# Performance work log

Hardware: AMD Instinct MI355X
Metric: run time of the kernel (lower is better)

The kernel has to match this reference:

```python
import jax, jax.numpy as jnp
import numpy as np

VS = 0.4
SENT = np.int32(2_000_000_000)  # > max lin code (1000^3)
EPS = 1e-5


def setup_inputs() -> dict:
    key = jax.random.key(0)
    ks = jax.random.split(key, 16)
    B, N, Cin, Cout = 8, 65536, 16, 128
    xyz = jax.random.uniform(ks[0], (B, N, 3), jnp.float32) * 51.2  # 128^3 voxel grid @ 0.4m
    feat = jax.random.normal(ks[1], (B, N, Cin), jnp.float32)
    mask = (jax.random.uniform(ks[2], (B, N)) < 0.9).astype(jnp.float32)
    def conv_w(k, ci, co):
        return jax.random.normal(k, (27, ci, co), jnp.float32) * (1.0 / np.sqrt(27.0 * ci))
    return {
        'xyz': xyz, 'feat': feat, 'mask': mask,
        'W1': conv_w(ks[3], Cin, 32), 'b1': jnp.zeros((32,), jnp.float32),
        'g1': jnp.ones((32,), jnp.float32), 'be1': jnp.zeros((32,), jnp.float32),
        'W2': conv_w(ks[4], 32, 64), 'b2': jnp.zeros((64,), jnp.float32),
        'g2': jnp.ones((64,), jnp.float32), 'be2': jnp.zeros((64,), jnp.float32),
        'W3': conv_w(ks[5], 64, Cout), 'b3': jnp.zeros((Cout,), jnp.float32),
        'g3': jnp.ones((Cout,), jnp.float32), 'be3': jnp.zeros((Cout,), jnp.float32),
    }


def _voxelize(lin_b, f_b, m_b):
    # sort-based unique with inverse; fixed capacity N slots (sentinel-padded)
    N = lin_b.shape[0]
    order = jnp.argsort(lin_b)
    s = lin_b[order]
    isnew = jnp.concatenate([jnp.ones((1,), bool), s[1:] != s[:-1]])
    rank = (jnp.cumsum(isnew) - 1).astype(jnp.int32)
    inv = jnp.zeros_like(lin_b).at[order].set(rank)          # point -> voxel slot
    unq = jnp.full_like(lin_b, SENT).at[rank].set(s)         # sorted unique codes, sentinel fill
    fsum = jax.ops.segment_sum(f_b * m_b[:, None], inv, num_segments=N)
    cnt = jnp.clip(jax.ops.segment_sum(m_b, inv, num_segments=N), 1.0)
    return unq, inv, fsum / cnt[:, None]


def _subm_conv(vfeat, unq, valid, W, b):
    # submanifold 3x3x3 conv on active voxels; neighbor lookup via binary search in sorted codes
    B, N, _ = vfeat.shape
    x = unq % 1000
    y = (unq // 1000) % 1000
    z = unq // 1000000
    brow = jnp.arange(B)[:, None]
    out = jnp.zeros((B, N, W.shape[-1]), vfeat.dtype)
    for ko in range(27):
        dz, dy, dx = ko // 9 - 1, (ko // 3) % 3 - 1, ko % 3 - 1
        ncode = unq + dx + 1000 * dy + 1000000 * dz
        inb = ((x + dx >= 0) & (x + dx < 1000) & (y + dy >= 0) & (y + dy < 1000)
               & (z + dz >= 0) & (z + dz < 1000))
        idx = jnp.clip(jax.vmap(jnp.searchsorted)(unq, ncode), 0, N - 1)
        found = (jnp.take_along_axis(unq, idx, 1) == ncode) & inb & valid
        nf = vfeat[brow, idx] * found[..., None].astype(vfeat.dtype)
        out = out + nf @ W[ko]
    return (out + b) * valid[..., None].astype(vfeat.dtype)


def _bn_relu(xv, g, be, valid):
    # BatchNorm1d (training stats) over valid voxel rows only, then ReLU
    w = valid[..., None].astype(xv.dtype)
    n = jnp.maximum(w.sum(), 1.0)
    mean = (xv * w).sum((0, 1)) / n
    var = (((xv - mean) ** 2) * w).sum((0, 1)) / n
    yv = (xv - mean) * jax.lax.rsqrt(var + EPS) * g + be
    return jax.nn.relu(yv) * w


def reference(xyz, feat, mask, W1, b1, g1, be1, W2, b2, g2, be2, W3, b3, g3, be3):
    B, N, _ = feat.shape
    origin = xyz.reshape(-1, 3).min(0)
    v = jnp.clip(((xyz - origin) / VS).astype(jnp.int32), 0, None)   # [B,N,3]
    lin = v[..., 0] + 1000 * (v[..., 1] + 1000 * v[..., 2])          # [B,N]
    unq, inv, vfeat = jax.vmap(_voxelize)(lin, feat, mask)
    valid = unq < SENT
    h = _bn_relu(_subm_conv(vfeat, unq, valid, W1, b1), g1, be1, valid)
    h = _bn_relu(_subm_conv(h, unq, valid, W2, b2), g2, be2, valid)
    h = _bn_relu(_subm_conv(h, unq, valid, W3, b3), g3, be3, valid)
    # scatter voxel features back to points (exact match: inv maps point -> its voxel slot)
    out_f = h[jnp.arange(B)[:, None], inv]                           # [B,N,Cout]
    return out_f * mask[..., None]
```

## Files before the change

kernel.cpp:

```cpp
#include <hip/hip_runtime.h>

#define NPTS   65536
#define NBATCH 8
#define TSIZE  131072
#define TM1    (TSIZE - 1)
#define CAP    8192
#define PPB    64
#define BMW    65536
#define STG    64
#define PCS    16

__device__ __forceinline__ unsigned hashf(int code) {
    unsigned u = (unsigned)code * 2654435761u;
    return (u >> 13) & TM1;
}

__global__ void init_origin(int* ob) {
    if (threadIdx.x < 3) ob[threadIdx.x] = 0x7F800000;
}

__global__ void minred(const float* __restrict__ xyz, int* __restrict__ ob) {
    int tid = threadIdx.x;
    float mx = INFINITY, my = INFINITY, mz = INFINITY;
    size_t total = (size_t)NBATCH * NPTS;
    for (size_t i = (size_t)blockIdx.x * blockDim.x + tid; i < total;
         i += (size_t)gridDim.x * blockDim.x) {
        mx = fminf(mx, xyz[i * 3 + 0]);
        my = fminf(my, xyz[i * 3 + 1]);
        mz = fminf(mz, xyz[i * 3 + 2]);
    }
    __shared__ float sx[256], sy[256], sz[256];
    sx[tid] = mx; sy[tid] = my; sz[tid] = mz;
    __syncthreads();
    for (int s = 128; s > 0; s >>= 1) {
        if (tid < s) {
            sx[tid] = fminf(sx[tid], sx[tid + s]);
            sy[tid] = fminf(sy[tid], sy[tid + s]);
            sz[tid] = fminf(sz[tid], sz[tid + s]);
        }
        __syncthreads();
    }
    if (tid == 0) {
        atomicMin(&ob[0], __float_as_int(sx[0]));
        atomicMin(&ob[1], __float_as_int(sy[0]));
        atomicMin(&ob[2], __float_as_int(sz[0]));
    }
}

__global__ void build_codes(const float* __restrict__ xyz, const int* __restrict__ ob,
                            int* __restrict__ pslot, int* __restrict__ hashk,
                            int* __restrict__ scnt) {
    int b = blockIdx.y;
    int p = blockIdx.x * blockDim.x + threadIdx.x;
    size_t gi = (size_t)b * NPTS + p;
    float ox = __int_as_float(ob[0]);
    float oy = __int_as_float(ob[1]);
    float oz = __int_as_float(ob[2]);
    float x = xyz[gi * 3 + 0], y = xyz[gi * 3 + 1], z = xyz[gi * 3 + 2];
    int vx = (int)((x - ox) / 0.4f); if (vx < 0) vx = 0;
    int vy = (int)((y - oy) / 0.4f); if (vy < 0) vy = 0;
    int vz = (int)((z - oz) / 0.4f); if (vz < 0) vz = 0;
    int code = vx | (vy << 7) | (vz << 14);
    int* hk = hashk + (size_t)b * TSIZE;
    unsigned s = hashf(code);
    while (true) {
        int prev = atomicCAS(&hk[s], -1, code);
        if (prev == -1 || prev == code) break;
        s = (s + 1) & TM1;
    }
    pslot[gi] = (int)s;
    atomicAdd(&scnt[(size_t)b * TSIZE + s], 1);
}

__global__ void assign_ids(const int* __restrict__ hashk, int* __restrict__ hashv,
                           int* __restrict__ nvox, int* __restrict__ voxcode,
                           unsigned* __restrict__ bitmap, const int* __restrict__ scnt,
                           int* __restrict__ vnpts) {
    int b = blockIdx.y;
    int s = blockIdx.x * blockDim.x + threadIdx.x;
    int k = hashk[(size_t)b * TSIZE + s];
    if (k != -1) {
        int id = atomicAdd(&nvox[b], 1);
        hashv[(size_t)b * TSIZE + s] = id;
        voxcode[(size_t)b * NPTS + id] = k;
        vnpts[(size_t)b * NPTS + id] = scnt[(size_t)b * TSIZE + s];
        atomicOr(&bitmap[(size_t)b * BMW + (k >> 5)], 1u << (k & 31));
    }
}

__global__ void point_pass(const int* __restrict__ pslot, const int* __restrict__ scnt,
                           const int* __restrict__ hashv, const float* __restrict__ feat,
                           const float* __restrict__ mask, int* __restrict__ inv,
                           float* __restrict__ cntf, float* __restrict__ fsum) {
    int b = blockIdx.y;
    int p = blockIdx.x * blockDim.x + threadIdx.x;
    size_t gi = (size_t)b * NPTS + p;
    int s = pslot[gi];
    int v = hashv[(size_t)b * TSIZE + s];
    inv[gi] = v;
    int n = scnt[(size_t)b * TSIZE + s];
    float m = mask[gi];
    const float4* f4 = (const float4*)(feat + gi * 16);
    float4 f0 = f4[0], f1 = f4[1], f2 = f4[2], f3 = f4[3];
    float* fs = fsum + ((size_t)b * NPTS + v) * 16;
    if (n == 1) {
        float4 o0 = {f0.x * m, f0.y * m, f0.z * m, f0.w * m};
        float4 o1 = {f1.x * m, f1.y * m, f1.z * m, f1.w * m};
        float4 o2 = {f2.x * m, f2.y * m, f2.z * m, f2.w * m};
        float4 o3 = {f3.x * m, f3.y * m, f3.z * m, f3.w * m};
        float4* fs4 = (float4*)fs;
        fs4[0] = o0; fs4[1] = o1; fs4[2] = o2; fs4[3] = o3;
    } else {
        atomicAdd(&cntf[(size_t)b * NPTS + v], m);
        atomicAdd(&fs[0],  f0.x * m); atomicAdd(&fs[1],  f0.y * m);
        atomicAdd(&fs[2],  f0.z * m); atomicAdd(&fs[3],  f0.w * m);
        atomicAdd(&fs[4],  f1.x * m); atomicAdd(&fs[5],  f1.y * m);
        atomicAdd(&fs[6],  f1.z * m); atomicAdd(&fs[7],  f1.w * m);
        atomicAdd(&fs[8],  f2.x * m); atomicAdd(&fs[9],  f2.y * m);
        atomicAdd(&fs[10], f2.z * m); atomicAdd(&fs[11], f2.w * m);
        atomicAdd(&fs[12], f3.x * m); atomicAdd(&fs[13], f3.y * m);
        atomicAdd(&fs[14], f3.z * m); atomicAdd(&fs[15], f3.w * m);
    }
}

__global__ void vfeat_div(float* __restrict__ fsum, const float* __restrict__ cntf,
                          const int* __restrict__ vnpts, const int* __restrict__ nvox) {
    int b = blockIdx.y;
    int v = blockIdx.x * blockDim.x + threadIdx.x;
    if (v >= nvox[b]) return;
    if (vnpts[(size_t)b * NPTS + v] <= 1) return;
    float cn = fmaxf(cntf[(size_t)b * NPTS + v], 1.0f);
    float* fs = fsum + ((size_t)b * NPTS + v) * 16;
    #pragma unroll
    for (int c = 0; c < 16; c++) fs[c] /= cn;
}

__global__ __launch_bounds__(256) void build_pairs(
    const int* __restrict__ hashk, const int* __restrict__ hashv,
    const int* __restrict__ voxcode, const int* __restrict__ nvox,
    const unsigned* __restrict__ bitmap,
    unsigned* __restrict__ pairs, int* __restrict__ paircnt) {
    int b = blockIdx.y;
    int t = threadIdx.x;
    int v = blockIdx.x * 256 + t;
    __shared__ int lcnt[32];
    __shared__ int lbase[32];
    __shared__ unsigned s_pay[27 * STG];
    if (t < 32) lcnt[t] = 0;
    __syncthreads();

    bool active = (v < nvox[b]);
    int code = 0;
    if (active) code = voxcode[(size_t)b * NPTS + v];
    int x = code & 127, y = (code >> 7) & 127, z = code >> 14;
    const unsigned* bm = bitmap + (size_t)b * BMW;
    const int* hk = hashk + (size_t)b * TSIZE;
    const int* hv = hashv + (size_t)b * TSIZE;

    int ncode[13];
    unsigned hitmask = 0;
    #pragma unroll
    for (int d = 0; d < 13; d++) {
        int dz = d / 9 - 1, r9 = d % 9;
        int dy = r9 / 3 - 1, dx = r9 % 3 - 1;
        int nx = x + dx, ny = y + dy, nz = z + dz;
        bool inb = active && ((unsigned)nx <= 127u) && ((unsigned)ny <= 127u) &&
                   ((unsigned)nz <= 127u);
        int nc = nx | (ny << 7) | (nz << 14);
        ncode[d] = nc;
        unsigned w = 0;
        if (inb) w = bm[nc >> 5];
        if (inb && ((w >> (nc & 31)) & 1u)) hitmask |= 1u << d;
    }

    #pragma unroll
    for (int d = 0; d < 13; d++) {
        if (hitmask & (1u << d)) {
            int nc = ncode[d];
            unsigned s = hashf(nc);
            int nb = -1;
            while (true) {
                int k = hk[s];
                if (k == nc) { nb = hv[s]; break; }
                if (k == -1) break;
                s = (s + 1) & TM1;
            }
            if (nb >= 0) {
                unsigned p1 = ((unsigned)v << 16) | (unsigned)nb;
                unsigned p2 = ((unsigned)nb << 16) | (unsigned)v;
                int l1 = atomicAdd(&lcnt[d], 1);
                if (l1 < STG) {
                    s_pay[d * STG + l1] = p1;
                } else {
                    int gs = atomicAdd(&paircnt[(b * 27 + d) * PCS], 1);
                    if (gs < CAP) pairs[(size_t)(b * 27 + d) * CAP + gs] = p1;
                }
                int k2 = 26 - d;
                int l2 = atomicAdd(&lcnt[k2], 1);
                if (l2 < STG) {
                    s_pay[k2 * STG + l2] = p2;
                } else {
                    int gs = atomicAdd(&paircnt[(b * 27 + k2) * PCS], 1);
                    if (gs < CAP) pairs[(size_t)(b * 27 + k2) * CAP + gs] = p2;
                }
            }
        }
    }
    __syncthreads();

    if (t < 27) {
        int n = lcnt[t]; if (n > STG) n = STG;
        lbase[t] = (n > 0) ? atomicAdd(&paircnt[(b * 27 + t) * PCS], n) : 0;
    }
    __syncthreads();

    for (int k = t; k < 27 * STG; k += 256) {
        int bkt = k / STG, i = k % STG;
        int n = lcnt[bkt]; if (n > STG) n = STG;
        if (i < n) {
            int gs = lbase[bkt] + i;
            if (gs < CAP) pairs[(size_t)(b * 27 + bkt) * CAP + gs] = s_pay[k];
        }
    }
}

template <int Cin, int Cout, bool XFORM>
__global__ __launch_bounds__(256) void conv_center(
    const float* __restrict__ in, float* __restrict__ outp,
    const float* __restrict__ W13, const float* __restrict__ bias,
    const float* __restrict__ sc, const float* __restrict__ sh,
    const int* __restrict__ nvox) {
    constexpr int BR  = 64;
    constexpr int CT  = (Cout < 64) ? Cout : 64;
    constexpr int RG  = 256 / CT;
    constexpr int RPT = BR / RG;
    constexpr int J   = Cout / CT;
    int b = blockIdx.y;
    int nv = nvox[b];
    int v0 = blockIdx.x * BR;
    if (v0 >= nv) return;
    __shared__ __align__(16) float A_s[Cin][BR + 4];
    __shared__ __align__(16) float W_s[Cin * Cout];
    int t = threadIdx.x;
    for (int i4 = t; i4 < Cin * Cout / 4; i4 += 256)
        ((float4*)W_s)[i4] = ((const float4*)W13)[i4];
    const float* inb = in + (size_t)b * NPTS * Cin;
    for (int i4 = t; i4 < BR * Cin / 4; i4 += 256) {
        int lin = i4 * 4;
        int r = lin / Cin, ci = lin % Cin;
        float4 val = *(const float4*)&inb[(size_t)(v0 + r) * Cin + ci];
        if (XFORM) {
            val.x = fmaxf(val.x * sc[ci + 0] + sh[ci + 0], 0.0f);
            val.y = fmaxf(val.y * sc[ci + 1] + sh[ci + 1], 0.0f);
            val.z = fmaxf(val.z * sc[ci + 2] + sh[ci + 2], 0.0f);
            val.w = fmaxf(val.w * sc[ci + 3] + sh[ci + 3], 0.0f);
        }
        A_s[ci + 0][r] = val.x;
        A_s[ci + 1][r] = val.y;
        A_s[ci + 2][r] = val.z;
        A_s[ci + 3][r] = val.w;
    }
    __syncthreads();
    int c = t % CT;
    int r0 = (t / CT) * RPT;
    float acc[RPT][J];
    #pragma unroll
    for (int r = 0; r < RPT; r++)
        #pragma unroll
        for (int j = 0; j < J; j++) acc[r][j] = 0.0f;
    #pragma unroll 4
    for (int ci = 0; ci < Cin; ci++) {
        float4 a4[RPT / 4];
        #pragma unroll
        for (int k = 0; k < RPT / 4; k++)
            a4[k] = *(const float4*)&A_s[ci][r0 + 4 * k];
        float w[J];
        #pragma unroll
        for (int j = 0; j < J; j++) w[j] = W_s[ci * Cout + c + CT * j];
        #pragma unroll
        for (int k = 0; k < RPT / 4; k++) {
            #pragma unroll
            for (int j = 0; j < J; j++) {
                acc[4 * k + 0][j] += a4[k].x * w[j];
                acc[4 * k + 1][j] += a4[k].y * w[j];
                acc[4 * k + 2][j] += a4[k].z * w[j];
                acc[4 * k + 3][j] += a4[k].w * w[j];
            }
        }
    }
    float* ob = outp + (size_t)b * NPTS * Cout;
    #pragma unroll
    for (int r = 0; r < RPT; r++) {
        int row = v0 + r0 + r;
        if (row < nv) {
            #pragma unroll
            for (int j = 0; j < J; j++)
                ob[(size_t)row * Cout + c + CT * j] = acc[r][j] + bias[c + CT * j];
        }
    }
}

template <int Cin, int Cout, bool XFORM>
__global__ __launch_bounds__(256) void conv_off(
    const float* __restrict__ in, float* __restrict__ outp,
    const float* __restrict__ W, const float* __restrict__ sc,
    const float* __restrict__ sh, const unsigned* __restrict__ pairs,
    const int* __restrict__ paircnt) {
    constexpr int BR  = PPB;
    constexpr int CT  = (Cout < 64) ? Cout : 64;
    constexpr int RG  = 256 / CT;
    constexpr int RPT = BR / RG;
    constexpr int J   = Cout / CT;
    int bk = blockIdx.y;
    int ko = bk % 27;
    int b  = bk / 27;
    int cnt = paircnt[bk * PCS];
    if (cnt > CAP) cnt = CAP;
    int start = blockIdx.x * BR;
    if (start >= cnt) return;
    int nActive = cnt - start; if (nActive > BR) nActive = BR;
    __shared__ __align__(16) float A_s[Cin][BR + 4];
    __shared__ __align__(16) float W_s[Cin * Cout];
    __shared__ unsigned pr_s[BR];
    int t = threadIdx.x;
    const float* Wk = W + (size_t)ko * Cin * Cout;
    for (int i4 = t; i4 < Cin * Cout / 4; i4 += 256)
        ((float4*)W_s)[i4] = ((const float4*)Wk)[i4];
    const unsigned* pb = pairs + (size_t)bk * CAP + start;
    if (t < BR) pr_s[t] = pb[t];
    __syncthreads();
    const float* inb = in + (size_t)b * NPTS * Cin;
    for (int i4 = t; i4 < BR * Cin / 4; i4 += 256) {
        int lin = i4 * 4;
        int r = lin / Cin, ci = lin % Cin;
        int vin = (int)(pr_s[r] & 0xffffu);
        float4 val = *(const float4*)&inb[(size_t)vin * Cin + ci];
        if (XFORM) {
            val.x = fmaxf(val.x * sc[ci + 0] + sh[ci + 0], 0.0f);
            val.y = fmaxf(val.y * sc[ci + 1] + sh[ci + 1], 0.0f);
            val.z = fmaxf(val.z * sc[ci + 2] + sh[ci + 2], 0.0f);
            val.w = fmaxf(val.w * sc[ci + 3] + sh[ci + 3], 0.0f);
        }
        A_s[ci + 0][r] = val.x;
        A_s[ci + 1][r] = val.y;
        A_s[ci + 2][r] = val.z;
        A_s[ci + 3][r] = val.w;
    }
    __syncthreads();
    int c = t % CT;
    int r0 = (t / CT) * RPT;
    float acc[RPT][J];
    #pragma unroll
    for (int r = 0; r < RPT; r++)
        #pragma unroll
        for (int j = 0; j < J; j++) acc[r][j] = 0.0f;
    #pragma unroll 4
    for (int ci = 0; ci < Cin; ci++) {
        float4 a4[RPT / 4];
        #pragma unroll
        for (int k = 0; k < RPT / 4; k++)
            a4[k] = *(const float4*)&A_s[ci][r0 + 4 * k];
        float w[J];
        #pragma unroll
        for (int j = 0; j < J; j++) w[j] = W_s[ci * Cout + c + CT * j];
        #pragma unroll
        for (int k = 0; k < RPT / 4; k++) {
            #pragma unroll
            for (int j = 0; j < J; j++) {
                acc[4 * k + 0][j] += a4[k].x * w[j];
                acc[4 * k + 1][j] += a4[k].y * w[j];
                acc[4 * k + 2][j] += a4[k].z * w[j];
                acc[4 * k + 3][j] += a4[k].w * w[j];
            }
        }
    }
    float* ob = outp + (size_t)b * NPTS * Cout;
    #pragma unroll
    for (int r = 0; r < RPT; r++) {
        if (r0 + r < nActive) {
            int vout = (int)(pr_s[r0 + r] >> 16);
            #pragma unroll
            for (int j = 0; j < J; j++)
                atomicAdd(&ob[(size_t)vout * Cout + c + CT * j], acc[r][j]);
        }
    }
}

template <int C>
__global__ void bn_stats(const float* __restrict__ h, const int* __restrict__ nvox,
                         float* __restrict__ sums) {
    constexpr int RPB = 256 / C;
    int b = blockIdx.y;
    int nv = nvox[b];
    int tid = threadIdx.x;
    int c = tid % C;
    int r = tid / C;
    float s0 = 0.0f, s1 = 0.0f;
    for (int v = blockIdx.x * RPB + r; v < nv; v += gridDim.x * RPB) {
        float x = h[((size_t)b * NPTS + v) * C + c];
        s0 += x;
        s1 += x * x;
    }
    __shared__ float l0[256], l1[256];
    l0[tid] = s0; l1[tid] = s1;
    __syncthreads();
    for (int s = 128; s >= C; s >>= 1) {
        if (tid < s) { l0[tid] += l0[tid + s]; l1[tid] += l1[tid + s]; }
        __syncthreads();
    }
    if (tid < C) {
        atomicAdd(&sums[c], l0[tid]);
        atomicAdd(&sums[C + c], l1[tid]);
    }
}

template <int C>
__global__ void bn_finalize(const float* __restrict__ sums, const int* __restrict__ nvox,
                            const float* __restrict__ g, const float* __restrict__ be,
                            float* __restrict__ scale, float* __restrict__ shift) {
    int c = threadIdx.x;
    if (c >= C) return;
    float n = 0.0f;
    for (int b = 0; b < NBATCH; b++) n += (float)nvox[b];
    n = fmaxf(n, 1.0f);
    float mean = sums[c] / n;
    float var = sums[C + c] / n - mean * mean;
    float a = g[c] * rsqrtf(var + 1e-5f);
    scale[c] = a;
    shift[c] = be[c] - mean * a;
}

__global__ void out_gather(const float* __restrict__ h3, const int* __restrict__ inv,
                           const float* __restrict__ mask, const float* __restrict__ sc,
                           const float* __restrict__ sh, float* __restrict__ out) {
    int b = blockIdx.y;
    size_t i = (size_t)blockIdx.x * blockDim.x + threadIdx.x;
    int p = (int)(i >> 7);
    int c = (int)(i & 127);
    size_t gi = (size_t)b * NPTS + p;
    int v = inv[gi];
    float m = mask[gi];
    float x = h3[((size_t)b * NPTS + v) * 128 + c];
    x = fmaxf(x * sc[c] + sh[c], 0.0f);
    out[gi * 128 + c] = x * m;
}

extern "C" void kernel_launch(void* const* d_in, const int* in_sizes, int n_in,
                              void* d_out, int out_size, void* d_ws, size_t ws_size,
                              hipStream_t stream) {
    const float* xyz  = (const float*)d_in[0];
    const float* feat = (const float*)d_in[1];
    const float* mask = (const float*)d_in[2];
    const float* W1 = (const float*)d_in[3];
    const float* b1 = (const float*)d_in[4];
    const float* g1 = (const float*)d_in[5];
    const float* be1 = (const float*)d_in[6];
    const float* W2 = (const float*)d_in[7];
    const float* b2 = (const float*)d_in[8];
    const float* g2 = (const float*)d_in[9];
    const float* be2 = (const float*)d_in[10];
    const float* W3 = (const float*)d_in[11];
    const float* b3 = (const float*)d_in[12];
    const float* g3 = (const float*)d_in[13];
    const float* be3 = (const float*)d_in[14];
    float* out = (float*)d_out;

    char* ws = (char*)d_ws;
    size_t off = 0;
    auto alloc = [&](size_t bytes) {
        void* p = ws + off;
        off += (bytes + 255) & ~(size_t)255;
        return p;
    };
    int*      hashk   = (int*)alloc((size_t)NBATCH * TSIZE * 4);
    int*      hashv   = (int*)alloc((size_t)NBATCH * TSIZE * 4);
    int*      scnt    = (int*)alloc((size_t)NBATCH * TSIZE * 4);
    int*      nvox    = (int*)alloc(NBATCH * 4);
    int*      origin  = (int*)alloc(16);
    int*      pslot   = (int*)alloc((size_t)NBATCH * NPTS * 4);
    int*      voxcode = (int*)alloc((size_t)NBATCH * NPTS * 4);
    int*      vnpts   = (int*)alloc((size_t)NBATCH * NPTS * 4);
    int*      inv     = (int*)alloc((size_t)NBATCH * NPTS * 4);
    float*    cntf    = (float*)alloc((size_t)NBATCH * NPTS * 4);
    unsigned* pairs   = (unsigned*)alloc((size_t)NBATCH * 27 * CAP * 4);
    int*      paircnt = (int*)alloc((size_t)NBATCH * 27 * PCS * 4);
    unsigned* bitmap  = (unsigned*)alloc((size_t)NBATCH * BMW * 4);
    float*    bnsums  = (float*)alloc(256 * 4);
    float*    bnscale = (float*)alloc(128 * 4);
    float*    bnshift = (float*)alloc(128 * 4);
    float*    A       = (float*)alloc((size_t)NBATCH * NPTS * 64 * 4);
    float*    Bb      = (float*)alloc((size_t)NBATCH * NPTS * 128 * 4);

    hipMemsetAsync(hashk, 0xFF, (size_t)NBATCH * TSIZE * 4, stream);
    hipMemsetAsync(scnt, 0, (size_t)NBATCH * TSIZE * 4, stream);
    hipMemsetAsync(nvox, 0, NBATCH * 4, stream);
    hipMemsetAsync(cntf, 0, (size_t)NBATCH * NPTS * 4, stream);
    hipMemsetAsync(A, 0, (size_t)NBATCH * NPTS * 16 * 4, stream);
    hipMemsetAsync(paircnt, 0, (size_t)NBATCH * 27 * PCS * 4, stream);
    hipMemsetAsync(bitmap, 0, (size_t)NBATCH * BMW * 4, stream);
    init_origin<<<1, 64, 0, stream>>>(origin);

    minred<<<512, 256, 0, stream>>>(xyz, origin);
    build_codes<<<dim3(NPTS / 256, NBATCH), 256, 0, stream>>>(xyz, origin, pslot, hashk, scnt);
    assign_ids<<<dim3(TSIZE / 256, NBATCH), 256, 0, stream>>>(hashk, hashv, nvox, voxcode,
                                                              bitmap, scnt, vnpts);
    point_pass<<<dim3(NPTS / 256, NBATCH), 256, 0, stream>>>(pslot, scnt, hashv, feat, mask,
                                                             inv, cntf, A);
    vfeat_div<<<dim3(NPTS / 256, NBATCH), 256, 0, stream>>>(A, cntf, vnpts, nvox);

    build_pairs<<<dim3(NPTS / 256, NBATCH), 256, 0, stream>>>(hashk, hashv, voxcode,
                                                              nvox, bitmap, pairs, paircnt);

    dim3 cgrid(NPTS / 64, NBATCH);
    dim3 ogrid(CAP / PPB, NBATCH * 27);

    conv_center<16, 32, false><<<cgrid, 256, 0, stream>>>(A, Bb, W1 + 13 * 16 * 32, b1,
                                                          nullptr, nullptr, nvox);
    conv_off<16, 32, false><<<ogrid, 256, 0, stream>>>(A, Bb, W1, nullptr, nullptr,
                                                       pairs, paircnt);
    hipMemsetAsync(bnsums, 0, 256 * 4, stream);
    bn_stats<32><<<dim3(64, NBATCH), 256, 0, stream>>>(Bb, nvox, bnsums);
    bn_finalize<32><<<1, 128, 0, stream>>>(bnsums, nvox, g1, be1, bnscale, bnshift);

    conv_center<32, 64, true><<<cgrid, 256, 0, stream>>>(Bb, A, W2 + 13 * 32 * 64, b2,
                                                         bnscale, bnshift, nvox);
    conv_off<32, 64, true><<<ogrid, 256, 0, stream>>>(Bb, A, W2, bnscale, bnshift,
                                                      pairs, paircnt);
    hipMemsetAsync(bnsums, 0, 256 * 4, stream);
    bn_stats<64><<<dim3(64, NBATCH), 256, 0, stream>>>(A, nvox, bnsums);
    bn_finalize<64><<<1, 128, 0, stream>>>(bnsums, nvox, g2, be2, bnscale, bnshift);

    conv_center<64, 128, true><<<cgrid, 256, 0, stream>>>(A, Bb, W3 + 13 * 64 * 128, b3,
                                                          bnscale, bnshift, nvox);
    conv_off<64, 128, true><<<ogrid, 256, 0, stream>>>(A, Bb, W3, bnscale, bnshift,
                                                       pairs, paircnt);
    hipMemsetAsync(bnsums, 0, 256 * 4, stream);
    bn_stats<128><<<dim3(64, NBATCH), 256, 0, stream>>>(Bb, nvox, bnsums);
    bn_finalize<128><<<1, 128, 0, stream>>>(bnsums, nvox, g3, be3, bnscale, bnshift);

    out_gather<<<dim3(NPTS * 128 / 256, NBATCH), 256, 0, stream>>>(Bb, inv, mask, bnscale,
                                                                   bnshift, out);
}
```

Baseline: 1.759 ms.

## Split conv output columns across grid z, swizzle LDS, loop chunks with prefetch in conv_off

The conv kernels now take a COLS template parameter. Layer 3's 128 output channels are split into two column tiles launched via blockIdx.z, so each block keeps one accumulator column per thread and the work spreads over more blocks. The shared-memory activation tile uses an XOR swizzle on the row index to reduce LDS bank conflicts. conv_off processes several 64-pair chunks per block, loading weights once and prefetching the next chunk's gathered inputs into registers while computing the current one. The trade-offs are extra syncthreads, duplicated gathers for the split layer, and fewer blocks for the offset convs.

```diff
diff --git a/kernel.cpp b/kernel.cpp
--- a/kernel.cpp
+++ b/kernel.cpp
@@ -6,6 +6,7 @@
 #define TM1    (TSIZE - 1)
 #define CAP    8192
 #define PPB    64
+#define CPB    4
 #define BMW    65536
 #define STG    64
 #define PCS    16
@@ -224,26 +225,29 @@
     }
 }
 
-template <int Cin, int Cout, bool XFORM>
+template <int Cin, int Cout, int COLS, bool XFORM>
 __global__ __launch_bounds__(256) void conv_center(
     const float* __restrict__ in, float* __restrict__ outp,
     const float* __restrict__ W13, const float* __restrict__ bias,
     const float* __restrict__ sc, const float* __restrict__ sh,
     const int* __restrict__ nvox) {
     constexpr int BR  = 64;
-    constexpr int CT  = (Cout < 64) ? Cout : 64;
+    constexpr int CT  = COLS;
     constexpr int RG  = 256 / CT;
     constexpr int RPT = BR / RG;
-    constexpr int J   = Cout / CT;
     int b = blockIdx.y;
     int nv = nvox[b];
     int v0 = blockIdx.x * BR;
     if (v0 >= nv) return;
+    int colofs = blockIdx.z * COLS;
     __shared__ __align__(16) float A_s[Cin][BR + 4];
-    __shared__ __align__(16) float W_s[Cin * Cout];
+    __shared__ __align__(16) float W_s[Cin * COLS];
     int t = threadIdx.x;
-    for (int i4 = t; i4 < Cin * Cout / 4; i4 += 256)
-        ((float4*)W_s)[i4] = ((const float4*)W13)[i4];
+    for (int i4 = t; i4 < Cin * COLS / 4; i4 += 256) {
+        int lin = i4 * 4;
+        int ci = lin / COLS, cc = lin % COLS;
+        *(float4*)&W_s[lin] = *(const float4*)&W13[(size_t)ci * Cout + colofs + cc];
+    }
     const float* inb = in + (size_t)b * NPTS * Cin;
     for (int i4 = t; i4 < BR * Cin / 4; i4 += 256) {
         int lin = i4 * 4;
@@ -255,134 +259,145 @@
             val.z = fmaxf(val.z * sc[ci + 2] + sh[ci + 2], 0.0f);
             val.w = fmaxf(val.w * sc[ci + 3] + sh[ci + 3], 0.0f);
         }
-        A_s[ci + 0][r] = val.x;
-        A_s[ci + 1][r] = val.y;
-        A_s[ci + 2][r] = val.z;
-        A_s[ci + 3][r] = val.w;
+        A_s[ci + 0][r ^ ((ci + 0) & 28)] = val.x;
+        A_s[ci + 1][r ^ ((ci + 1) & 28)] = val.y;
+        A_s[ci + 2][r ^ ((ci + 2) & 28)] = val.z;
+        A_s[ci + 3][r ^ ((ci + 3) & 28)] = val.w;
     }
     __syncthreads();
     int c = t % CT;
     int r0 = (t / CT) * RPT;
-    float acc[RPT][J];
-    #pragma unroll
-    for (int r = 0; r < RPT; r++)
-        #pragma unroll
-        for (int j = 0; j < J; j++) acc[r][j] = 0.0f;
+    float acc[RPT];
+    #pragma unroll
+    for (int r = 0; r < RPT; r++) acc[r] = 0.0f;
     #pragma unroll 4
     for (int ci = 0; ci < Cin; ci++) {
-        float4 a4[RPT / 4];
-        #pragma unroll
-        for (int k = 0; k < RPT / 4; k++)
-            a4[k] = *(const float4*)&A_s[ci][r0 + 4 * k];
-        float w[J];
-        #pragma unroll
-        for (int j = 0; j < J; j++) w[j] = W_s[ci * Cout + c + CT * j];
+        int sw = ci & 28;
+        float w = W_s[ci * COLS + c];
         #pragma unroll
         for (int k = 0; k < RPT / 4; k++) {
-            #pragma unroll
-            for (int j = 0; j < J; j++) {
-                acc[4 * k + 0][j] += a4[k].x * w[j];
-                acc[4 * k + 1][j] += a4[k].y * w[j];
-                acc[4 * k + 2][j] += a4[k].z * w[j];
-                acc[4 * k + 3][j] += a4[k].w * w[j];
-            }
+            float4 a4 = *(const float4*)&A_s[ci][(r0 + 4 * k) ^ sw];
+            acc[4 * k + 0] += a4.x * w;
+            acc[4 * k + 1] += a4.y * w;
+            acc[4 * k + 2] += a4.z * w;
+            acc[4 * k + 3] += a4.w * w;
         }
     }
     float* ob = outp + (size_t)b * NPTS * Cout;
+    float bs = bias[colofs + c];
     #pragma unroll
     for (int r = 0; r < RPT; r++) {
         int row = v0 + r0 + r;
-        if (row < nv) {
-            #pragma unroll
-            for (int j = 0; j < J; j++)
-                ob[(size_t)row * Cout + c + CT * j] = acc[r][j] + bias[c + CT * j];
-        }
-    }
-}
-
-template <int Cin, int Cout, bool XFORM>
+        if (row < nv)
+            ob[(size_t)row * Cout + colofs + c] = acc[r] + bs;
+    }
+}
+
+template <int Cin, int Cout, int COLS, bool XFORM>
 __global__ __launch_bounds__(256) void conv_off(
     const float* __restrict__ in, float* __restrict__ outp,
     const float* __restrict__ W, const float* __restrict__ sc,
     const float* __restrict__ sh, const unsigned* __restrict__ pairs,
     const int* __restrict__ paircnt) {
     constexpr int BR  = PPB;
-    constexpr int CT  = (Cout < 64) ? Cout : 64;
+    constexpr int CT  = COLS;
     constexpr int RG  = 256 / CT;
     constexpr int RPT = BR / RG;
-    constexpr int J   = Cout / CT;
+    constexpr int NQ  = BR * Cin / (4 * 256);
     int bk = blockIdx.y;
     int ko = bk % 27;
     int b  = bk / 27;
     int cnt = paircnt[bk * PCS];
     if (cnt > CAP) cnt = CAP;
-    int start = blockIdx.x * BR;
-    if (start >= cnt) return;
-    int nActive = cnt - start; if (nActive > BR) nActive = BR;
+    int base = blockIdx.x * (BR * CPB);
+    if (base >= cnt) return;
+    int colofs = blockIdx.z * COLS;
     __shared__ __align__(16) float A_s[Cin][BR + 4];
-    __shared__ __align__(16) float W_s[Cin * Cout];
-    __shared__ unsigned pr_s[BR];
+    __shared__ __align__(16) float W_s[Cin * COLS];
+    __shared__ unsigned pr_s[BR * CPB];
     int t = threadIdx.x;
     const float* Wk = W + (size_t)ko * Cin * Cout;
-    for (int i4 = t; i4 < Cin * Cout / 4; i4 += 256)
-        ((float4*)W_s)[i4] = ((const float4*)Wk)[i4];
-    const unsigned* pb = pairs + (size_t)bk * CAP + start;
-    if (t < BR) pr_s[t] = pb[t];
-    __syncthreads();
+    for (int i4 = t; i4 < Cin * COLS / 4; i4 += 256) {
+        int lin = i4 * 4;
+        int ci = lin / COLS, cc = lin % COLS;
+        *(float4*)&W_s[lin] = *(const float4*)&Wk[(size_t)ci * Cout + colofs + cc];
+    }
+    const unsigned* pb = pairs + (size_t)bk * CAP;
+    for (int i = t; i < BR * CPB; i += 256)
+        pr_s[i] = (base + i < cnt) ? pb[base + i] : 0u;
+    __syncthreads();
+
     const float* inb = in + (size_t)b * NPTS * Cin;
-    for (int i4 = t; i4 < BR * Cin / 4; i4 += 256) {
-        int lin = i4 * 4;
-        int r = lin / Cin, ci = lin % Cin;
-        int vin = (int)(pr_s[r] & 0xffffu);
-        float4 val = *(const float4*)&inb[(size_t)vin * Cin + ci];
-        if (XFORM) {
-            val.x = fmaxf(val.x * sc[ci + 0] + sh[ci + 0], 0.0f);
-            val.y = fmaxf(val.y * sc[ci + 1] + sh[ci + 1], 0.0f);
-            val.z = fmaxf(val.z * sc[ci + 2] + sh[ci + 2], 0.0f);
-            val.w = fmaxf(val.w * sc[ci + 3] + sh[ci + 3], 0.0f);
-        }
-        A_s[ci + 0][r] = val.x;
-        A_s[ci + 1][r] = val.y;
-        A_s[ci + 2][r] = val.z;
-        A_s[ci + 3][r] = val.w;
-    }
-    __syncthreads();
+    float* ob = outp + (size_t)b * NPTS * Cout;
     int c = t % CT;
     int r0 = (t / CT) * RPT;
-    float acc[RPT][J];
-    #pragma unroll
-    for (int r = 0; r < RPT; r++)
+
+    int rr[NQ], cch[NQ];
+    #pragma unroll
+    for (int q = 0; q < NQ; q++) {
+        int lin = (t + q * 256) * 4;
+        rr[q]  = lin / Cin;
+        cch[q] = lin % Cin;
+    }
+    float4 stg[NQ];
+    #pragma unroll
+    for (int q = 0; q < NQ; q++) {
+        int vin = (int)(pr_s[rr[q]] & 0xffffu);
+        stg[q] = *(const float4*)&inb[(size_t)vin * Cin + cch[q]];
+    }
+
+    int nchunk = (cnt - base + BR - 1) / BR;
+    if (nchunk > CPB) nchunk = CPB;
+    for (int ch = 0; ch < nchunk; ch++) {
         #pragma unroll
-        for (int j = 0; j < J; j++) acc[r][j] = 0.0f;
-    #pragma unroll 4
-    for (int ci = 0; ci < Cin; ci++) {
-        float4 a4[RPT / 4];
+        for (int q = 0; q < NQ; q++) {
+            float4 val = stg[q];
+            int ci = cch[q], r = rr[q];
+            if (XFORM) {
+                val.x = fmaxf(val.x * sc[ci + 0] + sh[ci + 0], 0.0f);
+                val.y = fmaxf(val.y * sc[ci + 1] + sh[ci + 1], 0.0f);
+                val.z = fmaxf(val.z * sc[ci + 2] + sh[ci + 2], 0.0f);
+                val.w = fmaxf(val.w * sc[ci + 3] + sh[ci + 3], 0.0f);
+            }
+            A_s[ci + 0][r ^ ((ci + 0) & 28)] = val.x;
+            A_s[ci + 1][r ^ ((ci + 1) & 28)] = val.y;
+            A_s[ci + 2][r ^ ((ci + 2) & 28)] = val.z;
+            A_s[ci + 3][r ^ ((ci + 3) & 28)] = val.w;
+        }
+        __syncthreads();
+        if (ch + 1 < nchunk) {
+            #pragma unroll
+            for (int q = 0; q < NQ; q++) {
+                int vin = (int)(pr_s[(ch + 1) * BR + rr[q]] & 0xffffu);
+                stg[q] = *(const float4*)&inb[(size_t)vin * Cin + cch[q]];
+            }
+        }
+        float acc[RPT];
         #pragma unroll
-        for (int k = 0; k < RPT / 4; k++)
-            a4[k] = *(const float4*)&A_s[ci][r0 + 4 * k];
-        float w[J];
+        for (int r = 0; r < RPT; r++) acc[r] = 0.0f;
+        #pragma unroll 4
+        for (int ci = 0; ci < Cin; ci++) {
+            int sw = ci & 28;
+            float w = W_s[ci * COLS + c];
+            #pragma unroll
+            for (int k = 0; k < RPT / 4; k++) {
+                float4 a4 = *(const float4*)&A_s[ci][(r0 + 4 * k) ^ sw];
+                acc[4 * k + 0] += a4.x * w;
+                acc[4 * k + 1] += a4.y * w;
+                acc[4 * k + 2] += a4.z * w;
+                acc[4 * k + 3] += a4.w * w;
+            }
+        }
+        int nAct = cnt - (base + ch * BR);
+        if (nAct > BR) nAct = BR;
         #pragma unroll
-        for (int j = 0; j < J; j++) w[j] = W_s[ci * Cout + c + CT * j];
-        #pragma unroll
-        for (int k = 0; k < RPT / 4; k++) {
-            #pragma unroll
-            for (int j = 0; j < J; j++) {
-                acc[4 * k + 0][j] += a4[k].x * w[j];
-                acc[4 * k + 1][j] += a4[k].y * w[j];
-                acc[4 * k + 2][j] += a4[k].z * w[j];
-                acc[4 * k + 3][j] += a4[k].w * w[j];
+        for (int r = 0; r < RPT; r++) {
+            if (r0 + r < nAct) {
+                int vout = (int)(pr_s[ch * BR + r0 + r] >> 16);
+                atomicAdd(&ob[(size_t)vout * Cout + colofs + c], acc[r]);
             }
         }
-    }
-    float* ob = outp + (size_t)b * NPTS * Cout;
-    #pragma unroll
-    for (int r = 0; r < RPT; r++) {
-        if (r0 + r < nActive) {
-            int vout = (int)(pr_s[r0 + r] >> 16);
-            #pragma unroll
-            for (int j = 0; j < J; j++)
-                atomicAdd(&ob[(size_t)vout * Cout + c + CT * j], acc[r][j]);
-        }
+        __syncthreads();
     }
 }
 
@@ -511,29 +526,33 @@
     build_pairs<<<dim3(NPTS / 256, NBATCH), 256, 0, stream>>>(hashk, hashv, voxcode,
                                                               nvox, bitmap, pairs, paircnt);
 
-    dim3 cgrid(NPTS / 64, NBATCH);
-    dim3 ogrid(CAP / PPB, NBATCH * 27);
-
-    conv_center<16, 32, false><<<cgrid, 256, 0, stream>>>(A, Bb, W1 + 13 * 16 * 32, b1,
-                                                          nullptr, nullptr, nvox);
-    conv_off<16, 32, false><<<ogrid, 256, 0, stream>>>(A, Bb, W1, nullptr, nullptr,
-                                                       pairs, paircnt);
+    dim3 cgrid1(NPTS / 64, NBATCH, 1);
+    dim3 cgrid2(NPTS / 64, NBATCH, 1);
+    dim3 cgrid3(NPTS / 64, NBATCH, 2);
+    dim3 ogrid1(CAP / (PPB * CPB), NBATCH * 27, 1);
+    dim3 ogrid2(CAP / (PPB * CPB), NBATCH * 27, 1);
+    dim3 ogrid3(CAP / (PPB * CPB), NBATCH * 27, 2);
+
+    conv_center<16, 32, 32, false><<<cgrid1, 256, 0, stream>>>(A, Bb, W1 + 13 * 16 * 32, b1,
+                                                               nullptr, nullptr, nvox);
+    conv_off<16, 32, 32, false><<<ogrid1, 256, 0, stream>>>(A, Bb, W1, nullptr, nullptr,
+                                                            pairs, paircnt);
     hipMemsetAsync(bnsums, 0, 256 * 4, stream);
     bn_stats<32><<<dim3(64, NBATCH), 256, 0, stream>>>(Bb, nvox, bnsums);
     bn_finalize<32><<<1, 128, 0, stream>>>(bnsums, nvox, g1, be1, bnscale, bnshift);
 
-    conv_center<32, 64, true><<<cgrid, 256, 0, stream>>>(Bb, A, W2 + 13 * 32 * 64, b2,
-                                                         bnscale, bnshift, nvox);
-    conv_off<32, 64, true><<<ogrid, 256, 0, stream>>>(Bb, A, W2, bnscale, bnshift,
-                                                      pairs, paircnt);
+    conv_center<32, 64, 64, true><<<cgrid2, 256, 0, stream>>>(Bb, A, W2 + 13 * 32 * 64, b2,
+                                                              bnscale, bnshift, nvox);
+    conv_off<32, 64, 64, true><<<ogrid2, 256, 0, stream>>>(Bb, A, W2, bnscale, bnshift,
+                                                           pairs, paircnt);
     hipMemsetAsync(bnsums, 0, 256 * 4, stream);
     bn_stats<64><<<dim3(64, NBATCH), 256, 0, stream>>>(A, nvox, bnsums);
     bn_finalize<64><<<1, 128, 0, stream>>>(bnsums, nvox, g2, be2, bnscale, bnshift);
 
-    conv_center<64, 128, true><<<cgrid, 256, 0, stream>>>(A, Bb, W3 + 13 * 64 * 128, b3,
-                                                          bnscale, bnshift, nvox);
-    conv_off<64, 128, true><<<ogrid, 256, 0, stream>>>(A, Bb, W3, bnscale, bnshift,
-                                                       pairs, paircnt);
+    conv_center<64, 128, 64, true><<<cgrid3, 256, 0, stream>>>(A, Bb, W3 + 13 * 64 * 128, b3,
+                                                               bnscale, bnshift, nvox);
+    conv_off<64, 128, 64, true><<<ogrid3, 256, 0, stream>>>(A, Bb, W3, bnscale, bnshift,
+                                                            pairs, paircnt);
     hipMemsetAsync(bnsums, 0, 256 * 4, stream);
     bn_stats<128><<<dim3(64, NBATCH), 256, 0, stream>>>(Bb, nvox, bnsums);
     bn_finalize<128><<<1, 128, 0, stream>>>(bnsums, nvox, g3, be3, bnscale, bnshift);
```

After: 2.254 ms. +28.1%, slower.
